# Optimization experiments

Hardware: AMD Instinct MI355X
Metric: run time of the kernel (lower is better)

## Reference

```python
import jax, jax.numpy as jnp
import numpy as np

T, B, N_IN, N_OUT = 100, 32, 1024, 512
LR_LTP, LR_LTD = 1e-4, -1e-4
TAU_PRE, TAU_POST, DT = 20.0, 20.0, 1.0
W_MIN, W_MAX = 0.0, 1.0
SPIKE_PROB = 0.05


def setup_inputs() -> dict:
    key = jax.random.key(0)
    k1, k2, k3 = jax.random.split(key, 3)
    weight = jax.random.uniform(k1, (N_OUT, N_IN), dtype=jnp.float32)
    pre_spikes = (jax.random.uniform(k2, (T, B, N_IN)) < SPIKE_PROB).astype(jnp.float32)
    post_spikes = (jax.random.uniform(k3, (T, B, N_OUT)) < SPIKE_PROB).astype(jnp.float32)
    pre_trace = jnp.zeros((B, N_IN), jnp.float32)
    post_trace = jnp.zeros((B, N_OUT), jnp.float32)
    return {"weight": weight, "pre_spikes": pre_spikes, "post_spikes": post_spikes,
            "pre_trace": pre_trace, "post_trace": post_trace}


def reference(weight, pre_spikes, post_spikes, pre_trace, post_trace):
    # weight: [N_out, N_in]; pre_spikes: [T,B,N_in]; post_spikes: [T,B,N_out]
    decay_pre = jnp.exp(jnp.asarray(-DT / TAU_PRE, weight.dtype))
    decay_post = jnp.exp(jnp.asarray(-DT / TAU_POST, weight.dtype))
    # Soft bounds (w_max=1.0 > 0 -> w_max - w; w_min=0.0 not < 0 -> w)
    soft_ltp = W_MAX - weight
    soft_ltd = weight
    Bf = jnp.asarray(pre_spikes.shape[1], weight.dtype)

    def step(carry, xs):
        pre_tr, post_tr, dw = carry
        pre_s, post_s = xs  # [B,N_in], [B,N_out]
        pre_tr = pre_tr * decay_pre + pre_s
        post_tr = post_tr * decay_post + post_s
        # batch-mean of outer products -> [N_out, N_in]
        ltp_mean = jnp.einsum('bo,bi->oi', post_s, pre_tr) / Bf
        ltd_mean = jnp.einsum('bo,bi->oi', post_tr, pre_s) / Bf
        dw = dw + LR_LTP * soft_ltp * ltp_mean + LR_LTD * soft_ltd * ltd_mean
        return (pre_tr, post_tr, dw), None

    init = (pre_trace, post_trace, jnp.zeros_like(weight))
    (pre_tr, post_tr, delta_w), _ = jax.lax.scan(step, init, (pre_spikes, post_spikes))
    return delta_w, pre_tr, post_tr
```

## Files before the change

### kernel.cpp

```cpp
#include <hip/hip_runtime.h>

typedef unsigned short ushort;
typedef unsigned int uint;
typedef unsigned char uchar;
typedef long long i64;
typedef __attribute__((ext_vector_type(4))) float floatx4;

#define T_STEPS 100
#define BATCH   32
#define NIN     1024
#define NOUT    512

#define SEG      112
#define KPAD     (BATCH * SEG)
#define KSTRIDEB 3648
#define KS       16
#define KCHUNK   (KPAD / KS)
#define BK       32

#define LR_LTP  (1e-4f)
#define LR_LTD  (-1e-4f)
#define INV_B   (1.0f / 32.0f)
#define DECAY   0.951229424500714f
#define D28     0.246596963941607f
#define TCH     28
#define NCHUNK  4

#define OFF_PRE  (NOUT * NIN)
#define OFF_POST (OFF_PRE + BATCH * NIN)

#define B_PRST  0
#define B_PRTT  ((size_t)NIN * KSTRIDEB)
#define B_POST  ((size_t)2 * NIN * KSTRIDEB)
#define B_POTT  ((size_t)2 * NIN * KSTRIDEB + (size_t)NOUT * KSTRIDEB)
#define B_END   ((size_t)2 * (NIN + NOUT) * KSTRIDEB)
#define SLABU   (NOUT * NIN + 128)


static __device__ __forceinline__ uint pk4_fp8(float a, float b, float c, float d) {
    uint v = 0;
    v = __builtin_amdgcn_cvt_pk_fp8_f32(a, b, v, false);
    v = __builtin_amdgcn_cvt_pk_fp8_f32(c, d, v, true);
    return v;
}

static __device__ __forceinline__ ushort f2bf(float f) {
    union { float f; unsigned int u; } v; v.f = f;
    unsigned int r = (v.u + 0x7FFFu + ((v.u >> 16) & 1u)) >> 16;
    return (ushort)r;
}

__global__ __launch_bounds__(256) void stdp_traces_t(
    const float* __restrict__ pre_s,
    const float* __restrict__ post_s,
    const float* __restrict__ pre_tr0,
    const float* __restrict__ post_tr0,
    uchar* __restrict__ pre_s_t, uchar* __restrict__ pre_tr_t,
    uchar* __restrict__ post_s_t, uchar* __restrict__ post_tr_t,
    float* __restrict__ out)
{
    __shared__ uint Ls[64 * 33];
    __shared__ uint Lt[64 * 33];
    __shared__ float Eend[NCHUNK][64];

    const int chain = threadIdx.x & 63;
    const int c     = threadIdx.x >> 6;
    const int g     = blockIdx.x * 64 + chain;

    const float* src; const float* init;
    int id, stride, outoff;
    if (g < BATCH * NIN) {
        src = pre_s;  init = pre_tr0;
        id = g;               stride = BATCH * NIN;  outoff = OFF_PRE;
    } else {
        src = post_s; init = post_tr0;
        id = g - BATCH * NIN; stride = BATCH * NOUT; outoff = OFF_POST;
    }

    const int t0 = c * TCH;
    float x[TCH];
    #pragma unroll
    for (int m = 0; m < TCH; ++m)
        x[m] = (t0 + m < T_STEPS) ? src[(size_t)(t0 + m) * stride + id] : 0.f;

    uint sp[7];
    #pragma unroll
    for (int j = 0; j < 7; ++j)
        sp[j] = pk4_fp8(x[4*j], x[4*j+1], x[4*j+2], x[4*j+3]);

    float e = 0.f;
    #pragma unroll
    for (int m = 0; m < TCH; ++m) { e = e * DECAY + x[m]; x[m] = e; }
    Eend[c][chain] = e;
    __syncthreads();

    float C = init[id];
    for (int cc = 0; cc < c; ++cc) C = C * D28 + Eend[cc][chain];
    float p = C * DECAY;
    #pragma unroll
    for (int m = 0; m < TCH; ++m) { x[m] += p; p *= DECAY; }

    if (c == NCHUNK - 1) out[outoff + id] = x[15];

    #pragma unroll
    for (int j = 0; j < 7; ++j) {
        const uint tj = pk4_fp8(x[4*j], x[4*j+1], x[4*j+2], x[4*j+3]);
        Ls[chain * 33 + c * 7 + j] = sp[j];
        Lt[chain * 33 + c * 7 + j] = tj;
    }
    __syncthreads();

    const int id0 = blockIdx.x * 64;
    uchar *dS, *dT; int b0, ch0;
    if (id0 < BATCH * NIN) {
        b0 = id0 >> 10; ch0 = id0 & 1023; dS = pre_s_t;  dT = pre_tr_t;
    } else {
        const int idq = id0 - BATCH * NIN;
        b0 = idq >> 9;  ch0 = idq & 511;  dS = post_s_t; dT = post_tr_t;
    }
    #pragma unroll
    for (int j = 0; j < 4; ++j) {
        const int q = threadIdx.x + 256 * j;
        if (q < 896) {
            const int op = q >= 448;
            const int qq = q - op * 448;
            const int r  = qq / 7;
            const int cc = qq - r * 7;
            const uint* l = (op ? Lt : Ls) + r * 33 + cc * 4;
            const uint4 v = make_uint4(l[0], l[1], l[2], l[3]);
            uchar* gd = (op ? dT : dS) + (size_t)(ch0 + r) * KSTRIDEB + b0 * SEG + cc * 16;
            *(uint4*)gd = v;
        }
    }
}

__global__ __launch_bounds__(256) void stdp_gemm_dual(
    const uchar* __restrict__ post_s_t, const uchar* __restrict__ pre_tr_t,
    const uchar* __restrict__ post_tr_t, const uchar* __restrict__ pre_s_t,
    const float* __restrict__ wmat, ushort* __restrict__ Spart)
{
    __shared__ uchar AsP[128 * 32];
    __shared__ uchar AsD[128 * 32];
    __shared__ uchar BsP[128 * 32];
    __shared__ uchar BsD[128 * 32];

    const int i0 = blockIdx.x * 128;
    const int o0 = blockIdx.y * 128;
    const int k0 = blockIdx.z * KCHUNK;

    const int tid  = threadIdx.x;
    const int w    = tid >> 6;
    const int lane = tid & 63;
    const int quad = lane >> 4;
    const int l16  = lane & 15;
    const int wm   = w & 1;
    const int wn   = w >> 1;

    floatx4 accP[4][4], accD[4][4];
    const floatx4 zero4 = {0.f, 0.f, 0.f, 0.f};
    #pragma unroll
    for (int mt = 0; mt < 4; ++mt)
        #pragma unroll
        for (int nt = 0; nt < 4; ++nt) { accP[mt][nt] = zero4; accD[mt][nt] = zero4; }

    for (int kb = k0; kb < k0 + KCHUNK; kb += BK) {
        {
            const int c   = w * 64 + lane;
            const int row = c >> 1;
            const int kob = (c & 1) * 16;
            const size_t aoff = (size_t)(o0 + row) * KSTRIDEB + kb + kob;
            const size_t boff = (size_t)(i0 + row) * KSTRIDEB + kb + kob;
            const int ldso = w * 1024;
            __builtin_amdgcn_global_load_lds(
                (const __attribute__((address_space(1))) void*)(post_s_t + aoff),
                (__attribute__((address_space(3))) void*)((char*)AsP + ldso), 16, 0, 0);
            __builtin_amdgcn_global_load_lds(
                (const __attribute__((address_space(1))) void*)(post_tr_t + aoff),
                (__attribute__((address_space(3))) void*)((char*)AsD + ldso), 16, 0, 0);
            __builtin_amdgcn_global_load_lds(
                (const __attribute__((address_space(1))) void*)(pre_tr_t + boff),
                (__attribute__((address_space(3))) void*)((char*)BsP + ldso), 16, 0, 0);
            __builtin_amdgcn_global_load_lds(
                (const __attribute__((address_space(1))) void*)(pre_s_t + boff),
                (__attribute__((address_space(3))) void*)((char*)BsD + ldso), 16, 0, 0);
        }
        __syncthreads();

        i64 aP[4], aD[4], bP[4], bD[4];
        #pragma unroll
        for (int mt = 0; mt < 4; ++mt) {
            const int r = (wm * 64 + mt * 16 + l16) * 32 + quad * 8;
            aP[mt] = *(const i64*)&AsP[r];
            aD[mt] = *(const i64*)&AsD[r];
        }
        #pragma unroll
        for (int nt = 0; nt < 4; ++nt) {
            const int r = (wn * 64 + nt * 16 + l16) * 32 + quad * 8;
            bP[nt] = *(const i64*)&BsP[r];
            bD[nt] = *(const i64*)&BsD[r];
        }
        #pragma unroll
        for (int mt = 0; mt < 4; ++mt)
            #pragma unroll
            for (int nt = 0; nt < 4; ++nt) {
                accP[mt][nt] = __builtin_amdgcn_mfma_f32_16x16x32_fp8_fp8(
                    aP[mt], bP[nt], accP[mt][nt], 0, 0, 0);
                accD[mt][nt] = __builtin_amdgcn_mfma_f32_16x16x32_fp8_fp8(
                    aD[mt], bD[nt], accD[mt][nt], 0, 0, 0);
            }
        __syncthreads();
    }

    ushort* Sz = Spart + (size_t)blockIdx.z * SLABU;
    const float c1 = LR_LTP * INV_B;
    const float c2 = LR_LTD * INV_B;
    #pragma unroll
    for (int mt = 0; mt < 4; ++mt) {
        const int obase = o0 + wm * 64 + mt * 16 + quad * 4;
        #pragma unroll
        for (int nt = 0; nt < 4; ++nt) {
            const int i = i0 + wn * 64 + nt * 16 + l16;
            #pragma unroll
            for (int r = 0; r < 4; ++r) {
                const size_t idx = (size_t)(obase + r) * NIN + i;
                const float wv = wmat[idx];
                const float v = c1 * (1.0f - wv) * accP[mt][nt][r]
                              + c2 * wv          * accD[mt][nt][r];
                Sz[idx] = f2bf(v);
            }
        }
    }
}

__global__ __launch_bounds__(128) void stdp_finalize(
    const ushort* __restrict__ Spart, float* __restrict__ out)
{
    const int j = blockIdx.x * blockDim.x + threadIdx.x;
    float s[8] = {0.f, 0.f, 0.f, 0.f, 0.f, 0.f, 0.f, 0.f};
    #pragma unroll
    for (int z = 0; z < KS; ++z) {
        const uint4 v = *(const uint4*)(Spart + (size_t)z * SLABU + (size_t)j * 8);
        const uint u[4] = {v.x, v.y, v.z, v.w};
        #pragma unroll
        for (int q = 0; q < 4; ++q) {
            union { uint u; float f; } lo, hi;
            lo.u = u[q] << 16;
            hi.u = u[q] & 0xFFFF0000u;
            s[2 * q]     += lo.f;
            s[2 * q + 1] += hi.f;
        }
    }
    float4* o = (float4*)(out + (size_t)j * 8);
    o[0] = make_float4(s[0], s[1], s[2], s[3]);
    o[1] = make_float4(s[4], s[5], s[6], s[7]);
}

extern "C" void kernel_launch(void* const* d_in, const int* in_sizes, int n_in,
                              void* d_out, int out_size, void* d_ws, size_t ws_size,
                              hipStream_t stream) {
    const float* weight   = (const float*)d_in[0];
    const float* pre_s    = (const float*)d_in[1];
    const float* post_s   = (const float*)d_in[2];
    const float* pre_tr0  = (const float*)d_in[3];
    const float* post_tr0 = (const float*)d_in[4];
    float* out = (float*)d_out;

    uchar* wsb = (uchar*)d_ws;
    uchar* pre_s_t   = wsb + B_PRST;
    uchar* pre_tr_t  = wsb + B_PRTT;
    uchar* post_s_t  = wsb + B_POST;
    uchar* post_tr_t = wsb + B_POTT;
    ushort* Spart    = (ushort*)(wsb + B_END);

    stdp_traces_t<<<dim3(BATCH * (NIN + NOUT) / 64), dim3(256), 0, stream>>>(
        pre_s, post_s, pre_tr0, post_tr0,
        pre_s_t, pre_tr_t, post_s_t, post_tr_t, out);

    stdp_gemm_dual<<<dim3(NIN / 128, NOUT / 128, KS), dim3(256), 0, stream>>>(
        post_s_t, pre_tr_t, post_tr_t, pre_s_t, weight, Spart);

    stdp_finalize<<<dim3((NOUT * NIN / 8) / 128), dim3(128), 0, stream>>>(
        Spart, out);
}
```

Before: 103.8 us.

## Switch to 32x32x64 scaled FP8 MFMA with direct global loads and 128-step segments

Replaces the 16x16x32 FP8 MFMA with the gfx950 scaled 32x32x64 f8f6f4 MFMA. Operands are now loaded straight from global memory into registers, so the LDS staging and the per-iteration barriers go away. The time chunk grows from 28 to 32 so each batch segment is 128 bytes and lines up with the 64-wide K step, and the transpose store loses its bounds check. The cost is more padding in K (zero work for t>=100), uncoalesced-ish direct global loads that depend on the cache, and a new accumulator layout in the epilogue.

```diff
diff --git a/kernel.cpp b/kernel.cpp
--- a/kernel.cpp
+++ b/kernel.cpp
@@ -3,27 +3,26 @@
 typedef unsigned short ushort;
 typedef unsigned int uint;
 typedef unsigned char uchar;
-typedef long long i64;
-typedef __attribute__((ext_vector_type(4))) float floatx4;
+typedef __attribute__((ext_vector_type(8))) int intx8;
+typedef __attribute__((ext_vector_type(16))) float floatx16;
 
 #define T_STEPS 100
 #define BATCH   32
 #define NIN     1024
 #define NOUT    512
 
-#define SEG      112
+#define SEG      128
 #define KPAD     (BATCH * SEG)
-#define KSTRIDEB 3648
+#define KSTRIDEB 4160
 #define KS       16
 #define KCHUNK   (KPAD / KS)
-#define BK       32
 
 #define LR_LTP  (1e-4f)
 #define LR_LTD  (-1e-4f)
 #define INV_B   (1.0f / 32.0f)
 #define DECAY   0.951229424500714f
-#define D28     0.246596963941607f
-#define TCH     28
+#define D32     0.201896517994655f
+#define TCH     32
 #define NCHUNK  4
 
 #define OFF_PRE  (NOUT * NIN)
@@ -83,9 +82,9 @@
     for (int m = 0; m < TCH; ++m)
         x[m] = (t0 + m < T_STEPS) ? src[(size_t)(t0 + m) * stride + id] : 0.f;
 
-    uint sp[7];
-    #pragma unroll
-    for (int j = 0; j < 7; ++j)
+    uint sp[8];
+    #pragma unroll
+    for (int j = 0; j < 8; ++j)
         sp[j] = pk4_fp8(x[4*j], x[4*j+1], x[4*j+2], x[4*j+3]);
 
     float e = 0.f;
@@ -95,18 +94,18 @@
     __syncthreads();
 
     float C = init[id];
-    for (int cc = 0; cc < c; ++cc) C = C * D28 + Eend[cc][chain];
+    for (int cc = 0; cc < c; ++cc) C = C * D32 + Eend[cc][chain];
     float p = C * DECAY;
     #pragma unroll
     for (int m = 0; m < TCH; ++m) { x[m] += p; p *= DECAY; }
 
-    if (c == NCHUNK - 1) out[outoff + id] = x[15];
-
-    #pragma unroll
-    for (int j = 0; j < 7; ++j) {
+    if (c == NCHUNK - 1) out[outoff + id] = x[3];
+
+    #pragma unroll
+    for (int j = 0; j < 8; ++j) {
         const uint tj = pk4_fp8(x[4*j], x[4*j+1], x[4*j+2], x[4*j+3]);
-        Ls[chain * 33 + c * 7 + j] = sp[j];
-        Lt[chain * 33 + c * 7 + j] = tj;
+        Ls[chain * 33 + c * 8 + j] = sp[j];
+        Lt[chain * 33 + c * 8 + j] = tj;
     }
     __syncthreads();
 
@@ -120,30 +119,32 @@
     }
     #pragma unroll
     for (int j = 0; j < 4; ++j) {
-        const int q = threadIdx.x + 256 * j;
-        if (q < 896) {
-            const int op = q >= 448;
-            const int qq = q - op * 448;
-            const int r  = qq / 7;
-            const int cc = qq - r * 7;
-            const uint* l = (op ? Lt : Ls) + r * 33 + cc * 4;
-            const uint4 v = make_uint4(l[0], l[1], l[2], l[3]);
-            uchar* gd = (op ? dT : dS) + (size_t)(ch0 + r) * KSTRIDEB + b0 * SEG + cc * 16;
-            *(uint4*)gd = v;
-        }
-    }
-}
-
-__global__ __launch_bounds__(256) void stdp_gemm_dual(
+        const int q  = threadIdx.x + 256 * j;
+        const int op = q >> 9;
+        const int qq = q & 511;
+        const int r  = qq >> 3;
+        const int cc = qq & 7;
+        const uint* l = (op ? Lt : Ls) + r * 33 + cc * 4;
+        const uint4 v = make_uint4(l[0], l[1], l[2], l[3]);
+        uchar* gd = (op ? dT : dS) + (size_t)(ch0 + r) * KSTRIDEB + b0 * SEG + cc * 16;
+        *(uint4*)gd = v;
+    }
+}
+
+static __device__ __forceinline__ intx8 ld32(const uchar* p) {
+    const uint4 lo = *(const uint4*)p;
+    const uint4 hv = *(const uint4*)(p + 16);
+    intx8 r;
+    r[0] = (int)lo.x; r[1] = (int)lo.y; r[2] = (int)lo.z; r[3] = (int)lo.w;
+    r[4] = (int)hv.x; r[5] = (int)hv.y; r[6] = (int)hv.z; r[7] = (int)hv.w;
+    return r;
+}
+
+__global__ __launch_bounds__(256, 2) void stdp_gemm_dual(
     const uchar* __restrict__ post_s_t, const uchar* __restrict__ pre_tr_t,
     const uchar* __restrict__ post_tr_t, const uchar* __restrict__ pre_s_t,
     const float* __restrict__ wmat, ushort* __restrict__ Spart)
 {
-    __shared__ uchar AsP[128 * 32];
-    __shared__ uchar AsD[128 * 32];
-    __shared__ uchar BsP[128 * 32];
-    __shared__ uchar BsD[128 * 32];
-
     const int i0 = blockIdx.x * 128;
     const int o0 = blockIdx.y * 128;
     const int k0 = blockIdx.z * KCHUNK;
@@ -151,78 +152,63 @@
     const int tid  = threadIdx.x;
     const int w    = tid >> 6;
     const int lane = tid & 63;
-    const int quad = lane >> 4;
-    const int l16  = lane & 15;
     const int wm   = w & 1;
     const int wn   = w >> 1;
-
-    floatx4 accP[4][4], accD[4][4];
-    const floatx4 zero4 = {0.f, 0.f, 0.f, 0.f};
-    #pragma unroll
-    for (int mt = 0; mt < 4; ++mt)
-        #pragma unroll
-        for (int nt = 0; nt < 4; ++nt) { accP[mt][nt] = zero4; accD[mt][nt] = zero4; }
-
-    for (int kb = k0; kb < k0 + KCHUNK; kb += BK) {
-        {
-            const int c   = w * 64 + lane;
-            const int row = c >> 1;
-            const int kob = (c & 1) * 16;
-            const size_t aoff = (size_t)(o0 + row) * KSTRIDEB + kb + kob;
-            const size_t boff = (size_t)(i0 + row) * KSTRIDEB + kb + kob;
-            const int ldso = w * 1024;
-            __builtin_amdgcn_global_load_lds(
-                (const __attribute__((address_space(1))) void*)(post_s_t + aoff),
-                (__attribute__((address_space(3))) void*)((char*)AsP + ldso), 16, 0, 0);
-            __builtin_amdgcn_global_load_lds(
-                (const __attribute__((address_space(1))) void*)(post_tr_t + aoff),
-                (__attribute__((address_space(3))) void*)((char*)AsD + ldso), 16, 0, 0);
-            __builtin_amdgcn_global_load_lds(
-                (const __attribute__((address_space(1))) void*)(pre_tr_t + boff),
-                (__attribute__((address_space(3))) void*)((char*)BsP + ldso), 16, 0, 0);
-            __builtin_amdgcn_global_load_lds(
-                (const __attribute__((address_space(1))) void*)(pre_s_t + boff),
-                (__attribute__((address_space(3))) void*)((char*)BsD + ldso), 16, 0, 0);
-        }
-        __syncthreads();
-
-        i64 aP[4], aD[4], bP[4], bD[4];
-        #pragma unroll
-        for (int mt = 0; mt < 4; ++mt) {
-            const int r = (wm * 64 + mt * 16 + l16) * 32 + quad * 8;
-            aP[mt] = *(const i64*)&AsP[r];
-            aD[mt] = *(const i64*)&AsD[r];
-        }
-        #pragma unroll
-        for (int nt = 0; nt < 4; ++nt) {
-            const int r = (wn * 64 + nt * 16 + l16) * 32 + quad * 8;
-            bP[nt] = *(const i64*)&BsP[r];
-            bD[nt] = *(const i64*)&BsD[r];
-        }
-        #pragma unroll
-        for (int mt = 0; mt < 4; ++mt)
+    const int l32  = lane & 31;
+    const int hi   = lane >> 5;
+
+    floatx16 accP[2][2], accD[2][2];
+    #pragma unroll
+    for (int mt = 0; mt < 2; ++mt)
+        #pragma unroll
+        for (int nt = 0; nt < 2; ++nt)
             #pragma unroll
-            for (int nt = 0; nt < 4; ++nt) {
-                accP[mt][nt] = __builtin_amdgcn_mfma_f32_16x16x32_fp8_fp8(
-                    aP[mt], bP[nt], accP[mt][nt], 0, 0, 0);
-                accD[mt][nt] = __builtin_amdgcn_mfma_f32_16x16x32_fp8_fp8(
-                    aD[mt], bD[nt], accD[mt][nt], 0, 0, 0);
+            for (int r = 0; r < 16; ++r) {
+                accP[mt][nt][r] = 0.f; accD[mt][nt][r] = 0.f;
             }
-        __syncthreads();
+
+    const size_t aBase = (size_t)(o0 + wm * 64 + l32) * KSTRIDEB;
+    const size_t bBase = (size_t)(i0 + wn * 64 + l32) * KSTRIDEB;
+
+    for (int kb = k0; kb < k0 + KCHUNK; kb += 64) {
+        const int ko = kb + (hi << 5);
+        intx8 aP[2], aD[2], bP[2], bD[2];
+        #pragma unroll
+        for (int mt = 0; mt < 2; ++mt) {
+            const size_t off = aBase + (size_t)(mt * 32) * KSTRIDEB + ko;
+            aP[mt] = ld32(post_s_t  + off);
+            aD[mt] = ld32(post_tr_t + off);
+        }
+        #pragma unroll
+        for (int nt = 0; nt < 2; ++nt) {
+            const size_t off = bBase + (size_t)(nt * 32) * KSTRIDEB + ko;
+            bP[nt] = ld32(pre_tr_t + off);
+            bD[nt] = ld32(pre_s_t  + off);
+        }
+        #pragma unroll
+        for (int mt = 0; mt < 2; ++mt)
+            #pragma unroll
+            for (int nt = 0; nt < 2; ++nt) {
+                accP[mt][nt] = __builtin_amdgcn_mfma_scale_f32_32x32x64_f8f6f4(
+                    aP[mt], bP[nt], accP[mt][nt], 0, 0, 0, 127, 0, 127);
+                accD[mt][nt] = __builtin_amdgcn_mfma_scale_f32_32x32x64_f8f6f4(
+                    aD[mt], bD[nt], accD[mt][nt], 0, 0, 0, 127, 0, 127);
+            }
     }
 
     ushort* Sz = Spart + (size_t)blockIdx.z * SLABU;
     const float c1 = LR_LTP * INV_B;
     const float c2 = LR_LTD * INV_B;
     #pragma unroll
-    for (int mt = 0; mt < 4; ++mt) {
-        const int obase = o0 + wm * 64 + mt * 16 + quad * 4;
-        #pragma unroll
-        for (int nt = 0; nt < 4; ++nt) {
-            const int i = i0 + wn * 64 + nt * 16 + l16;
+    for (int mt = 0; mt < 2; ++mt) {
+        const int ob = o0 + wm * 64 + mt * 32 + hi * 4;
+        #pragma unroll
+        for (int nt = 0; nt < 2; ++nt) {
+            const int i = i0 + wn * 64 + nt * 32 + l32;
             #pragma unroll
-            for (int r = 0; r < 4; ++r) {
-                const size_t idx = (size_t)(obase + r) * NIN + i;
+            for (int r = 0; r < 16; ++r) {
+                const int o = ob + (r & 3) + 8 * (r >> 2);
+                const size_t idx = (size_t)o * NIN + i;
                 const float wv = wmat[idx];
                 const float v = c1 * (1.0f - wv) * accP[mt][nt][r]
                               + c2 * wv          * accD[mt][nt][r];
```

Result: faster. 100.5 us (-3.1%).
